# Kernel tuning notes

Hardware: AMD Instinct MI355X
Metric: run time of the kernel (lower is better)

Reference implementation:

```python
import jax, jax.numpy as jnp
import numpy as np

EPS = 1e-12  # F.normalize default eps


def _l2norm(x, axis):
    n = jnp.sqrt(jnp.sum(x * x, axis=axis, keepdims=True))
    return x / jnp.maximum(n, EPS)


def setup_inputs() -> dict:
    key = jax.random.key(0)
    k1, k2, k3, k4 = jax.random.split(key, 4)
    N, T, C, K = 64, 577, 768, 64
    return {
        "grids": jax.random.normal(k1, (N, T, C), dtype=jnp.float32),
        "conv_w": jax.random.normal(k2, (K, C), dtype=jnp.float32) * 0.03,
        "conv_b": jax.random.normal(k3, (K,), dtype=jnp.float32) * 0.01,
        "centroids": jax.random.normal(k4, (K, C), dtype=jnp.float32) * 0.03,
    }


def reference(grids, conv_w, conv_b, centroids):
    # grids: (N, 577, 768) -> (N, C=768, T=577), matching view+permute in torch
    N = grids.shape[0]
    x = jnp.transpose(grids.reshape(N, 577, 768), (0, 2, 1))  # (N, C, T)
    # per-token L2 normalization over channel dim
    x = _l2norm(x, axis=1)
    # 1x1 conv == per-token linear: (N, K, T)
    logits = jnp.einsum('kc,nct->nkt', conv_w, x) + conv_b[None, :, None]
    a = jax.nn.softmax(logits, axis=1)  # softmax over regions K
    # NetVLAD algebraic rewrite of sum_t a[n,k,t]*(x[n,:,t]-c[k,:]):
    #   = (a @ x^T)[n,k,c] - sum_t(a)[n,k] * c[k,c]
    p = jnp.einsum('nkt,nct->nkc', a, x) - a.sum(axis=-1)[:, :, None] * centroids[None]
    p = _l2norm(p, axis=2)             # intra-region normalization
    p = p.reshape(N, -1)               # (N, K*C)
    p = _l2norm(p, axis=1)             # global normalization
    return p
```

## Files before the change

kernel.cpp:

```cpp
#include <hip/hip_runtime.h>
#include <hip/hip_bf16.h>
#include <math.h>

#define TT 577
#define TP 640
#define CCH 768
#define KR 64
#define NB 64

typedef __attribute__((ext_vector_type(8))) short bf16x8;
typedef __attribute__((ext_vector_type(8))) unsigned short ushort8;
typedef __attribute__((ext_vector_type(4))) float f32x4;

static constexpr float EPSF = 1e-12f;

static __device__ inline unsigned short f2bf(float f) {
    return __bfloat16_as_ushort(__float2bfloat16(f));
}

__global__ __launch_bounds__(256) void k_prep(
    const float* __restrict__ conv_w,
    unsigned short* __restrict__ ws_w,
    unsigned short* __restrict__ ws_a)
{
    const int g = blockIdx.x * 256 + threadIdx.x;
    if (g < 6144) {
        const float* s = conv_w + (size_t)g * 8;
        float4 v0 = *reinterpret_cast<const float4*>(s);
        float4 v1 = *reinterpret_cast<const float4*>(s + 4);
        ushort8 o;
        o[0]=f2bf(v0.x); o[1]=f2bf(v0.y); o[2]=f2bf(v0.z); o[3]=f2bf(v0.w);
        o[4]=f2bf(v1.x); o[5]=f2bf(v1.y); o[6]=f2bf(v1.z); o[7]=f2bf(v1.w);
        *reinterpret_cast<ushort8*>(ws_w + (size_t)g * 8) = o;
    }
    if (g < 4096) {
        unsigned short* d = ws_a + (size_t)g * TP + 592;
        ushort8 z = {0,0,0,0,0,0,0,0};
        #pragma unroll
        for (int i = 0; i < 6; ++i)
            *reinterpret_cast<ushort8*>(d + i * 8) = z;
    }
}

__global__ __launch_bounds__(256, 3) void k_logits(
    const float* __restrict__ grids,
    const unsigned short* __restrict__ ws_w,
    const float* __restrict__ conv_b,
    unsigned short* __restrict__ ws_a,
    float* __restrict__ ws_asum)
{
    __shared__ __align__(16) unsigned short Wl[2][KR * 136];
    __shared__ float asum_lds[4][64];

    const int tid  = threadIdx.x;
    const int lane = tid & 63;
    const int w    = tid >> 6;
    const int n    = blockIdx.x / 10;
    const int tb   = (blockIdx.x - n * 10) << 6;
    const int t0w  = tb + (w << 4);

    const int lr = lane & 15;
    const int lg = lane >> 4;

    const int tokA = t0w + lr;
    const bool validA = (tokA < TT);
    const float* gsrc = grids + ((size_t)n * TT + tokA) * CCH + (lg << 3);

    ushort8 wreg0, wreg1, wreg2, wreg3;
    #define WLOAD(c0_)                                                         \
        {                                                                      \
            const int u0_ = tid,       u1_ = tid + 256,                        \
                      u2_ = tid + 512, u3_ = tid + 768;                        \
            wreg0 = *reinterpret_cast<const ushort8*>(                         \
                ws_w + (size_t)(u0_ >> 4) * CCH + (c0_) + ((u0_ & 15) << 3));  \
            wreg1 = *reinterpret_cast<const ushort8*>(                         \
                ws_w + (size_t)(u1_ >> 4) * CCH + (c0_) + ((u1_ & 15) << 3));  \
            wreg2 = *reinterpret_cast<const ushort8*>(                         \
                ws_w + (size_t)(u2_ >> 4) * CCH + (c0_) + ((u2_ & 15) << 3));  \
            wreg3 = *reinterpret_cast<const ushort8*>(                         \
                ws_w + (size_t)(u3_ >> 4) * CCH + (c0_) + ((u3_ & 15) << 3));  \
        }
    #define WSTORE(buf_)                                                       \
        {                                                                      \
            const int u0_ = tid,       u1_ = tid + 256,                        \
                      u2_ = tid + 512, u3_ = tid + 768;                        \
            *reinterpret_cast<ushort8*>(                                       \
                &Wl[buf_][(u0_ >> 4) * 136 + ((u0_ & 15) << 3)]) = wreg0;      \
            *reinterpret_cast<ushort8*>(                                       \
                &Wl[buf_][(u1_ >> 4) * 136 + ((u1_ & 15) << 3)]) = wreg1;      \
            *reinterpret_cast<ushort8*>(                                       \
                &Wl[buf_][(u2_ >> 4) * 136 + ((u2_ & 15) << 3)]) = wreg2;      \
            *reinterpret_cast<ushort8*>(                                       \
                &Wl[buf_][(u3_ >> 4) * 136 + ((u3_ & 15) << 3)]) = wreg3;      \
        }

    f32x4 acc[4] = {};
    float ss = 0.f;

    WLOAD(0)
    WSTORE(0)
    __syncthreads();

    for (int ch = 0; ch < 6; ++ch) {
        if (ch < 5) WLOAD((ch + 1) << 7)
        const int c0 = ch << 7;
        const unsigned short* Wb = Wl[ch & 1];

        #pragma unroll
        for (int s = 0; s < 4; ++s) {
            float a8[8];
            if (validA) {
                float4 u0 = *reinterpret_cast<const float4*>(gsrc + c0 + (s << 5));
                float4 u1 = *reinterpret_cast<const float4*>(gsrc + c0 + (s << 5) + 4);
                a8[0]=u0.x; a8[1]=u0.y; a8[2]=u0.z; a8[3]=u0.w;
                a8[4]=u1.x; a8[5]=u1.y; a8[6]=u1.z; a8[7]=u1.w;
            } else {
                #pragma unroll
                for (int j = 0; j < 8; ++j) a8[j] = 0.f;
            }
            bf16x8 afrag;
            #pragma unroll
            for (int j = 0; j < 8; ++j) {
                ss = fmaf(a8[j], a8[j], ss);
                ((unsigned short*)&afrag)[j] = f2bf(a8[j]);
            }
            const int cl = (s << 5) + (lg << 3);
            #pragma unroll
            for (int rt = 0; rt < 4; ++rt) {
                bf16x8 bfrag = *reinterpret_cast<const bf16x8*>(&Wb[(rt*16 + lr)*136 + cl]);
                acc[rt] = __builtin_amdgcn_mfma_f32_16x16x32_bf16(afrag, bfrag, acc[rt], 0, 0, 0);
            }
        }

        if (ch < 5) WSTORE((ch + 1) & 1)
        __syncthreads();
    }

    ss += __shfl_xor(ss, 16);
    ss += __shfl_xor(ss, 32);
    const float nrm = sqrtf(ss);
    const float inv = 1.0f / fmaxf(nrm, EPSF);

    float b_[4];
    #pragma unroll
    for (int rt = 0; rt < 4; ++rt) b_[rt] = conv_b[rt*16 + lr];

    float invT[4];
    #pragma unroll
    for (int reg = 0; reg < 4; ++reg) invT[reg] = __shfl(inv, (lg << 2) + reg);

    float lgt[4][4], mx[4];
    #pragma unroll
    for (int reg = 0; reg < 4; ++reg) {
        float m = -1e30f;
        #pragma unroll
        for (int rt = 0; rt < 4; ++rt) {
            lgt[rt][reg] = fmaf(acc[rt][reg], invT[reg], b_[rt]);
            m = fmaxf(m, lgt[rt][reg]);
        }
        mx[reg] = m;
    }
    #pragma unroll
    for (int msk = 1; msk < 16; msk <<= 1) {
        #pragma unroll
        for (int reg = 0; reg < 4; ++reg) mx[reg] = fmaxf(mx[reg], __shfl_xor(mx[reg], msk));
    }
    float ex[4][4], sm[4] = {0.f, 0.f, 0.f, 0.f};
    #pragma unroll
    for (int rt = 0; rt < 4; ++rt) {
        #pragma unroll
        for (int reg = 0; reg < 4; ++reg) {
            ex[rt][reg] = __expf(lgt[rt][reg] - mx[reg]);
            sm[reg] += ex[rt][reg];
        }
    }
    #pragma unroll
    for (int msk = 1; msk < 16; msk <<= 1) {
        #pragma unroll
        for (int reg = 0; reg < 4; ++reg) sm[reg] += __shfl_xor(sm[reg], msk);
    }

    float rsm[4];
    #pragma unroll
    for (int reg = 0; reg < 4; ++reg) {
        const bool vt = (t0w + (lg << 2) + reg) < TT;
        rsm[reg] = vt ? (1.0f / sm[reg]) : 0.f;
    }

    float pa[4];
    #pragma unroll
    for (int rt = 0; rt < 4; ++rt) {
        pa[rt] = ex[rt][0]*rsm[0] + ex[rt][1]*rsm[1] + ex[rt][2]*rsm[2] + ex[rt][3]*rsm[3];
        pa[rt] += __shfl_xor(pa[rt], 16);
        pa[rt] += __shfl_xor(pa[rt], 32);
    }
    if (lane < 16) {
        #pragma unroll
        for (int rt = 0; rt < 4; ++rt)
            asum_lds[w][rt*16 + lane] = pa[rt];
    }

    unsigned short* Abuf = &Wl[0][0] + (size_t)w * KR * 24;
    #pragma unroll
    for (int reg = 0; reg < 4; ++reg) {
        const int trow = (lg << 2) + reg;
        const float scale = invT[reg] * rsm[reg];
        #pragma unroll
        for (int rt = 0; rt < 4; ++rt)
            Abuf[(rt*16 + lr)*24 + trow] = f2bf(ex[rt][reg] * scale);
    }
    __syncthreads();

    if (tid < 64)
        ws_asum[(size_t)blockIdx.x * 64 + tid] =
            asum_lds[0][tid] + asum_lds[1][tid] + asum_lds[2][tid] + asum_lds[3][tid];

    {
        ushort8 r0 = *reinterpret_cast<const ushort8*>(&Abuf[lane * 24]);
        ushort8 r1 = *reinterpret_cast<const ushort8*>(&Abuf[lane * 24 + 8]);
        unsigned short* dst = ws_a + ((size_t)n * KR + lane) * TP + t0w;
        *reinterpret_cast<ushort8*>(dst)     = r0;
        *reinterpret_cast<ushort8*>(dst + 8) = r1;
    }
}

#define LOADA(d0,d1,d2,d3,t0_)                                                   \
    d0 = *reinterpret_cast<const bf16x8*>(abase +           (size_t)(t0_));      \
    d1 = *reinterpret_cast<const bf16x8*>(abase + 16*TP +   (size_t)(t0_));      \
    d2 = *reinterpret_cast<const bf16x8*>(abase + 32*TP +   (size_t)(t0_));      \
    d3 = *reinterpret_cast<const bf16x8*>(abase + 48*TP +   (size_t)(t0_));

#define LOADB(d,t0_) do {                                                        \
    const int tb2_ = (t0_) + (lg << 3);                                          \
    if ((t0_) + 32 <= TT) {                                                      \
        _Pragma("unroll")                                                        \
        for (int j_ = 0; j_ < 8; ++j_)                                           \
            ((unsigned short*)&(d))[j_] = f2bf(gb[(size_t)(tb2_ + j_) * CCH]);   \
    } else {                                                                     \
        _Pragma("unroll")                                                        \
        for (int j_ = 0; j_ < 8; ++j_) {                                         \
            float v_ = (tb2_ + j_ < TT) ? gb[(size_t)(tb2_ + j_) * CCH] : 0.f;   \
            ((unsigned short*)&(d))[j_] = f2bf(v_);                              \
        }                                                                        \
    } } while (0)

__global__ __launch_bounds__(256, 4) void k_vlad(
    const float* __restrict__ grids,
    const unsigned short* __restrict__ ws_a,
    const float* __restrict__ ws_asum,
    const float* __restrict__ centroids,
    float* __restrict__ out)
{
    __shared__ float asum_s[64];

    const int tid  = threadIdx.x;
    const int lane = tid & 63;
    const int w    = tid >> 6;
    const int n    = blockIdx.x / 12;
    const int c0   = (blockIdx.x - n * 12) << 6;
    const int lr   = lane & 15;
    const int lg   = lane >> 4;

    if (tid < 64) {
        float s = 0.f;
        #pragma unroll
        for (int b = 0; b < 10; ++b)
            s += ws_asum[((size_t)n * 10 + b) * 64 + tid];
        asum_s[tid] = s;
    }
    __syncthreads();

    const int c = c0 + (w << 4) + lr;
    const unsigned short* abase = ws_a + ((size_t)n * KR + lr) * TP + (lg << 3);
    const float* gb = grids + (size_t)n * TT * CCH + c;

    f32x4 acc0 = {}, acc1 = {}, acc2 = {}, acc3 = {};
    bf16x8 a0, a1, a2, a3, b0;
    bf16x8 p0, p1, p2, p3, q0;

    LOADA(a0, a1, a2, a3, 0)
    LOADB(b0, 0);

    int t0 = 0;
    while (true) {
        int tn = t0 + 32;
        if (tn < TT) { LOADA(p0, p1, p2, p3, tn) LOADB(q0, tn); }
        acc0 = __builtin_amdgcn_mfma_f32_16x16x32_bf16(a0, b0, acc0, 0, 0, 0);
        acc1 = __builtin_amdgcn_mfma_f32_16x16x32_bf16(a1, b0, acc1, 0, 0, 0);
        acc2 = __builtin_amdgcn_mfma_f32_16x16x32_bf16(a2, b0, acc2, 0, 0, 0);
        acc3 = __builtin_amdgcn_mfma_f32_16x16x32_bf16(a3, b0, acc3, 0, 0, 0);
        t0 = tn;
        if (t0 >= TT) break;

        tn = t0 + 32;
        if (tn < TT) { LOADA(a0, a1, a2, a3, tn) LOADB(b0, tn); }
        acc0 = __builtin_amdgcn_mfma_f32_16x16x32_bf16(p0, q0, acc0, 0, 0, 0);
        acc1 = __builtin_amdgcn_mfma_f32_16x16x32_bf16(p1, q0, acc1, 0, 0, 0);
        acc2 = __builtin_amdgcn_mfma_f32_16x16x32_bf16(p2, q0, acc2, 0, 0, 0);
        acc3 = __builtin_amdgcn_mfma_f32_16x16x32_bf16(p3, q0, acc3, 0, 0, 0);
        t0 = tn;
        if (t0 >= TT) break;
    }

    #pragma unroll
    for (int reg = 0; reg < 4; ++reg) {
        {
            const int kr = 0*16 + (lg << 2) + reg;
            out[((size_t)n * KR + kr) * CCH + c] =
                acc0[reg] - asum_s[kr] * centroids[(size_t)kr * CCH + c];
        }
        {
            const int kr = 1*16 + (lg << 2) + reg;
            out[((size_t)n * KR + kr) * CCH + c] =
                acc1[reg] - asum_s[kr] * centroids[(size_t)kr * CCH + c];
        }
        {
            const int kr = 2*16 + (lg << 2) + reg;
            out[((size_t)n * KR + kr) * CCH + c] =
                acc2[reg] - asum_s[kr] * centroids[(size_t)kr * CCH + c];
        }
        {
            const int kr = 3*16 + (lg << 2) + reg;
            out[((size_t)n * KR + kr) * CCH + c] =
                acc3[reg] - asum_s[kr] * centroids[(size_t)kr * CCH + c];
        }
    }
}

__global__ __launch_bounds__(256) void kc_norm_kernel(float* __restrict__ out)
{
    const int tid = threadIdx.x;
    const int sub = tid >> 6;
    const int l   = tid & 63;
    float4* p = reinterpret_cast<float4*>(out) + ((size_t)blockIdx.x * 4 + sub) * 192;
    float4 v0 = p[l];
    float4 v1 = p[l + 64];
    float4 v2 = p[l + 128];
    float ss = v0.x*v0.x + v0.y*v0.y + v0.z*v0.z + v0.w*v0.w
             + v1.x*v1.x + v1.y*v1.y + v1.z*v1.z + v1.w*v1.w
             + v2.x*v2.x + v2.y*v2.y + v2.z*v2.z + v2.w*v2.w;
    #pragma unroll
    for (int m = 1; m < 64; m <<= 1) ss += __shfl_xor(ss, m);
    const float sc = 0.125f / fmaxf(sqrtf(ss), EPSF);
    v0.x*=sc; v0.y*=sc; v0.z*=sc; v0.w*=sc;
    v1.x*=sc; v1.y*=sc; v1.z*=sc; v1.w*=sc;
    v2.x*=sc; v2.y*=sc; v2.z*=sc; v2.w*=sc;
    p[l] = v0;
    p[l + 64] = v1;
    p[l + 128] = v2;
}

extern "C" void kernel_launch(void* const* d_in, const int* in_sizes, int n_in,
                              void* d_out, int out_size, void* d_ws, size_t ws_size,
                              hipStream_t stream)
{
    const float* grids     = (const float*)d_in[0];
    const float* conv_w    = (const float*)d_in[1];
    const float* conv_b    = (const float*)d_in[2];
    const float* centroids = (const float*)d_in[3];
    float* out = (float*)d_out;

    unsigned short* ws_a    = (unsigned short*)d_ws;
    float*          ws_asum = (float*)((char*)d_ws + 5242880);
    unsigned short* ws_w    = (unsigned short*)((char*)d_ws + 5406720);

    hipLaunchKernelGGL(k_prep, dim3(24), dim3(256), 0, stream,
                       conv_w, ws_w, ws_a);
    hipLaunchKernelGGL(k_logits, dim3(NB * 10), dim3(256), 0, stream,
                       grids, ws_w, conv_b, ws_a, ws_asum);
    hipLaunchKernelGGL(k_vlad, dim3(NB * 12), dim3(256), 0, stream,
                       grids, ws_a, ws_asum, centroids, out);
    hipLaunchKernelGGL(kc_norm_kernel, dim3(NB * KR / 4), dim3(256), 0, stream, out);
}
```

Measured before the change: 74.21 us.

## Stage grids tiles through LDS with coalesced loads in logits kernel

```diff
diff --git a/kernel.cpp b/kernel.cpp
--- a/kernel.cpp
+++ b/kernel.cpp
@@ -7,6 +7,7 @@
 #define CCH 768
 #define KR 64
 #define NB 64
+#define LSTR 136
 
 typedef __attribute__((ext_vector_type(8))) short bf16x8;
 typedef __attribute__((ext_vector_type(8))) unsigned short ushort8;
@@ -16,6 +17,10 @@
 
 static __device__ inline unsigned short f2bf(float f) {
     return __bfloat16_as_ushort(__float2bfloat16(f));
+}
+static __device__ inline float bf2f(unsigned short b) {
+    union { unsigned int u; float f; } v; v.u = ((unsigned int)b) << 16;
+    return v.f;
 }
 
 __global__ __launch_bounds__(256) void k_prep(
@@ -49,7 +54,8 @@
     unsigned short* __restrict__ ws_a,
     float* __restrict__ ws_asum)
 {
-    __shared__ __align__(16) unsigned short Wl[2][KR * 136];
+    __shared__ __align__(16) unsigned short Gs[2][64 * LSTR];
+    __shared__ __align__(16) unsigned short Ws[64 * LSTR];
     __shared__ float asum_lds[4][64];
 
     const int tid  = threadIdx.x;
@@ -62,78 +68,86 @@
     const int lr = lane & 15;
     const int lg = lane >> 4;
 
-    const int tokA = t0w + lr;
-    const bool validA = (tokA < TT);
-    const float* gsrc = grids + ((size_t)n * TT + tokA) * CCH + (lg << 3);
-
-    ushort8 wreg0, wreg1, wreg2, wreg3;
-    #define WLOAD(c0_)                                                         \
-        {                                                                      \
-            const int u0_ = tid,       u1_ = tid + 256,                        \
-                      u2_ = tid + 512, u3_ = tid + 768;                        \
-            wreg0 = *reinterpret_cast<const ushort8*>(                         \
-                ws_w + (size_t)(u0_ >> 4) * CCH + (c0_) + ((u0_ & 15) << 3));  \
-            wreg1 = *reinterpret_cast<const ushort8*>(                         \
-                ws_w + (size_t)(u1_ >> 4) * CCH + (c0_) + ((u1_ & 15) << 3));  \
-            wreg2 = *reinterpret_cast<const ushort8*>(                         \
-                ws_w + (size_t)(u2_ >> 4) * CCH + (c0_) + ((u2_ & 15) << 3));  \
-            wreg3 = *reinterpret_cast<const ushort8*>(                         \
-                ws_w + (size_t)(u3_ >> 4) * CCH + (c0_) + ((u3_ & 15) << 3));  \
-        }
-    #define WSTORE(buf_)                                                       \
-        {                                                                      \
-            const int u0_ = tid,       u1_ = tid + 256,                        \
-                      u2_ = tid + 512, u3_ = tid + 768;                        \
-            *reinterpret_cast<ushort8*>(                                       \
-                &Wl[buf_][(u0_ >> 4) * 136 + ((u0_ & 15) << 3)]) = wreg0;      \
-            *reinterpret_cast<ushort8*>(                                       \
-                &Wl[buf_][(u1_ >> 4) * 136 + ((u1_ & 15) << 3)]) = wreg1;      \
-            *reinterpret_cast<ushort8*>(                                       \
-                &Wl[buf_][(u2_ >> 4) * 136 + ((u2_ & 15) << 3)]) = wreg2;      \
-            *reinterpret_cast<ushort8*>(                                       \
-                &Wl[buf_][(u3_ >> 4) * 136 + ((u3_ & 15) << 3)]) = wreg3;      \
-        }
+    const float* gbase = grids + (size_t)n * TT * CCH;
+
+    float4  ga[8];
+    ushort8 wa[4];
+
+    #define GLOAD(c0_)                                                        \
+        { _Pragma("unroll")                                                   \
+          for (int it = 0; it < 8; ++it) {                                    \
+              const int f = (it << 8) + tid;                                  \
+              const int t = f >> 5, c4 = f & 31;                              \
+              ga[it] = (tb + t < TT)                                          \
+                  ? *reinterpret_cast<const float4*>(                         \
+                        gbase + (size_t)(tb + t) * CCH + (c0_) + (c4 << 2))   \
+                  : make_float4(0.f, 0.f, 0.f, 0.f);                          \
+          } }
+
+    #define GWRITE(buf_)                                                      \
+        { _Pragma("unroll")                                                   \
+          for (int it = 0; it < 8; ++it) {                                    \
+              const int f = (it << 8) + tid;                                  \
+              const int t = f >> 5, c4 = f & 31;                              \
+              unsigned short o4[4] = { f2bf(ga[it].x), f2bf(ga[it].y),        \
+                                       f2bf(ga[it].z), f2bf(ga[it].w) };      \
+              *reinterpret_cast<uint2*>(&Gs[buf_][t * LSTR + (c4 << 2)]) =    \
+                  *reinterpret_cast<const uint2*>(o4);                        \
+          } }
+
+    #define WLOADD(c0_)                                                       \
+        { _Pragma("unroll")                                                   \
+          for (int it = 0; it < 4; ++it) {                                    \
+              const int f = (it << 8) + tid;                                  \
+              const int kr = f >> 4, c8 = f & 15;                             \
+              wa[it] = *reinterpret_cast<const ushort8*>(                     \
+                  ws_w + (size_t)kr * CCH + (c0_) + (c8 << 3));               \
+          } }
+
+    #define WWRITED()                                                         \
+        { _Pragma("unroll")                                                   \
+          for (int it = 0; it < 4; ++it) {                                    \
+              const int f = (it << 8) + tid;                                  \
+              const int kr = f >> 4, c8 = f & 15;                             \
+              *reinterpret_cast<ushort8*>(&Ws[kr * LSTR + (c8 << 3)]) = wa[it]; \
+          } }
 
     f32x4 acc[4] = {};
     float ss = 0.f;
 
-    WLOAD(0)
-    WSTORE(0)
+    GLOAD(0) WLOADD(0)
+    GWRITE(0) WWRITED()
     __syncthreads();
 
     for (int ch = 0; ch < 6; ++ch) {
-        if (ch < 5) WLOAD((ch + 1) << 7)
-        const int c0 = ch << 7;
-        const unsigned short* Wb = Wl[ch & 1];
-
+        if (ch < 5) { GLOAD((ch + 1) << 7) WLOADD((ch + 1) << 7) }
+
+        const unsigned short* Gb = &Gs[ch & 1][0];
         #pragma unroll
         for (int s = 0; s < 4; ++s) {
-            float a8[8];
-            if (validA) {
-                float4 u0 = *reinterpret_cast<const float4*>(gsrc + c0 + (s << 5));
-                float4 u1 = *reinterpret_cast<const float4*>(gsrc + c0 + (s << 5) + 4);
-                a8[0]=u0.x; a8[1]=u0.y; a8[2]=u0.z; a8[3]=u0.w;
-                a8[4]=u1.x; a8[5]=u1.y; a8[6]=u1.z; a8[7]=u1.w;
-            } else {
-                #pragma unroll
-                for (int j = 0; j < 8; ++j) a8[j] = 0.f;
-            }
-            bf16x8 afrag;
+            const int cl = (s << 5) + (lg << 3);
+            bf16x8 af = *reinterpret_cast<const bf16x8*>(
+                &Gb[((w << 4) + lr) * LSTR + cl]);
             #pragma unroll
             for (int j = 0; j < 8; ++j) {
-                ss = fmaf(a8[j], a8[j], ss);
-                ((unsigned short*)&afrag)[j] = f2bf(a8[j]);
+                const float v = bf2f(((unsigned short*)&af)[j]);
+                ss = fmaf(v, v, ss);
             }
-            const int cl = (s << 5) + (lg << 3);
-            #pragma unroll
-            for (int rt = 0; rt < 4; ++rt) {
-                bf16x8 bfrag = *reinterpret_cast<const bf16x8*>(&Wb[(rt*16 + lr)*136 + cl]);
-                acc[rt] = __builtin_amdgcn_mfma_f32_16x16x32_bf16(afrag, bfrag, acc[rt], 0, 0, 0);
-            }
-        }
-
-        if (ch < 5) WSTORE((ch + 1) & 1)
-        __syncthreads();
+            bf16x8 b0 = *reinterpret_cast<const bf16x8*>(&Ws[ lr        * LSTR + cl]);
+            bf16x8 b1 = *reinterpret_cast<const bf16x8*>(&Ws[(16 + lr) * LSTR + cl]);
+            bf16x8 b2 = *reinterpret_cast<const bf16x8*>(&Ws[(32 + lr) * LSTR + cl]);
+            bf16x8 b3 = *reinterpret_cast<const bf16x8*>(&Ws[(48 + lr) * LSTR + cl]);
+            acc[0] = __builtin_amdgcn_mfma_f32_16x16x32_bf16(af, b0, acc[0], 0, 0, 0);
+            acc[1] = __builtin_amdgcn_mfma_f32_16x16x32_bf16(af, b1, acc[1], 0, 0, 0);
+            acc[2] = __builtin_amdgcn_mfma_f32_16x16x32_bf16(af, b2, acc[2], 0, 0, 0);
+            acc[3] = __builtin_amdgcn_mfma_f32_16x16x32_bf16(af, b3, acc[3], 0, 0, 0);
+        }
+
+        if (ch < 5) {
+            __syncthreads();
+            GWRITE((ch + 1) & 1) WWRITED()
+            __syncthreads();
+        }
     }
 
     ss += __shfl_xor(ss, 16);
@@ -200,7 +214,7 @@
             asum_lds[w][rt*16 + lane] = pa[rt];
     }
 
-    unsigned short* Abuf = &Wl[0][0] + (size_t)w * KR * 24;
+    unsigned short* Abuf = &Gs[0][0] + (size_t)w * KR * 24;
     #pragma unroll
     for (int reg = 0; reg < 4; ++reg) {
         const int trow = (lg << 2) + reg;
```

After: 78.83 us. +6.2%, slower.
